# Optimization experiments

Hardware: AMD Instinct MI355X
Metric: run time of the kernel (lower is better)

Reference implementation:

```python
import jax, jax.numpy as jnp
import numpy as np

B, N = 2048, 64
Q_SIZE, K_SIZE, HIDDEN, OUT_SIZE, N_HEAD = 512, 512, 128, 512, 8
LN_EPS = 1e-5


def setup_inputs() -> dict:
    key = jax.random.key(0)
    ks = jax.random.split(key, 9)
    s_q = 1.0 / np.sqrt(Q_SIZE)
    s_k = 1.0 / np.sqrt(K_SIZE)
    s_o = 1.0 / np.sqrt(N_HEAD * HIDDEN)
    return {
        "me": jax.random.normal(ks[0], (B, Q_SIZE), jnp.float32),
        "other": jax.random.normal(ks[1], (B, N, K_SIZE), jnp.float32),
        # stacked per-head projection weights (torch Linear applied as x @ W)
        "Wq": jax.random.normal(ks[2], (N_HEAD, Q_SIZE, HIDDEN), jnp.float32) * s_q,
        "bq": jnp.zeros((N_HEAD, HIDDEN), jnp.float32),
        "Wk": jax.random.normal(ks[3], (N_HEAD, K_SIZE, HIDDEN), jnp.float32) * s_k,
        "Wv": jax.random.normal(ks[4], (N_HEAD, K_SIZE, HIDDEN), jnp.float32) * s_k,
        "gamma": jnp.ones((N_HEAD * HIDDEN,), jnp.float32),
        "beta": jnp.zeros((N_HEAD * HIDDEN,), jnp.float32),
        "Wo": jax.random.normal(ks[5], (N_HEAD * HIDDEN, OUT_SIZE), jnp.float32) * s_o,
    }


def _mhat2(me, other, Wq, bq, Wk, Wv, gamma, beta, Wo):
    # per-head projections, batched over the head axis
    q = jnp.einsum("bq,hqd->bhd", me, Wq) + bq[None]          # [B,H,D]
    k = jnp.einsum("bnk,hkd->bhnd", other, Wk)                 # [B,H,N,D]
    v = jnp.einsum("bnk,hkd->bhnd", other, Wv)                 # [B,H,N,D]
    scale = 1.0 / jnp.sqrt(jnp.asarray(HIDDEN, me.dtype))
    a = jnp.einsum("bhd,bhnd->bhn", q, k) * scale              # [B,H,N]
    a = jax.nn.softmax(a, axis=-1)
    out = jnp.einsum("bhn,bhnd->bhd", a, v)                    # [B,H,D]
    c = out.reshape(out.shape[0], N_HEAD * HIDDEN)             # concat heads
    mu = jnp.mean(c, axis=-1, keepdims=True)
    var = jnp.mean(jnp.square(c - mu), axis=-1, keepdims=True)
    cn = (c - mu) * jax.lax.rsqrt(var + LN_EPS) * gamma + beta
    return jax.nn.relu(cn) @ Wo                                # [B,OUT]


def reference(me, other, Wq, bq, Wk, Wv, gamma, beta, Wo):
    return _mhat2(me, other, Wq, bq, Wk, Wv, gamma, beta, Wo)
```

## Files before the change

### kernel.cpp

```cpp
#include <hip/hip_runtime.h>
#include <math.h>

typedef __attribute__((ext_vector_type(4))) float f32x4;
typedef __attribute__((ext_vector_type(4))) unsigned int u32x4;
typedef __attribute__((ext_vector_type(8))) short s16x8;

#define SCALE_INV_SQRT_H 0.08838834764831845f

__device__ __forceinline__ unsigned short f2bf(float x){
  unsigned int u = __builtin_bit_cast(unsigned int, x);
  u += 0x7fffu + ((u >> 16) & 1u);
  return (unsigned short)(u >> 16);
}
__device__ __forceinline__ float bf2f(unsigned short s){
  unsigned int u = ((unsigned int)s) << 16;
  return __builtin_bit_cast(float, u);
}

__device__ __forceinline__ void gemm_core(
    const unsigned short* __restrict__ Ag, int lda,
    const unsigned short* __restrict__ Bg, int ldb,
    int ksteps, unsigned short* As, unsigned short* Bs, f32x4 acc[4][4])
{
  const int t = threadIdx.x, lane = t & 63, w = t >> 6;
  const int m0 = (w >> 1) * 64, n0 = (w & 1) * 64;
  const int r = t >> 1, u0 = (t & 1) * 4;
  for (int kk = 0; kk < ksteps; kk++) {
    __syncthreads();
    const unsigned short* ga = Ag + (size_t)r * lda + kk * 64;
    const unsigned short* gb = Bg + (size_t)r * ldb + kk * 64;
#pragma unroll
    for (int q = 0; q < 4; q++) {
      u32x4 va = *(const u32x4*)(ga + (u0 + q) * 8);
      u32x4 vb = *(const u32x4*)(gb + (u0 + q) * 8);
      ((u32x4*)(As + r * 64))[(u0 + q) ^ (r & 7)] = va;
      ((u32x4*)(Bs + r * 64))[(u0 + q) ^ (r & 7)] = vb;
    }
    __syncthreads();
    s16x8 af[4][2], bfr[4][2];
#pragma unroll
    for (int i = 0; i < 4; i++) {
#pragma unroll
      for (int ks = 0; ks < 2; ks++) {
        int ra = m0 + i * 16 + (lane & 15);
        int sa = ks * 4 + (lane >> 4);
        af[i][ks] = *(const s16x8*)(As + ra * 64 + ((sa ^ (ra & 7)) << 3));
        int rb = n0 + i * 16 + (lane & 15);
        bfr[i][ks] = *(const s16x8*)(Bs + rb * 64 + ((sa ^ (rb & 7)) << 3));
      }
    }
#pragma unroll
    for (int ks = 0; ks < 2; ks++)
#pragma unroll
      for (int i = 0; i < 4; i++)
#pragma unroll
        for (int j = 0; j < 4; j++)
          acc[i][j] = __builtin_amdgcn_mfma_f32_16x16x32_bf16(af[i][ks], bfr[j][ks], acc[i][j], 0, 0, 0);
  }
}

__device__ __forceinline__ void store_bf16_tile(unsigned short* __restrict__ C, int ldc, f32x4 acc[4][4]){
  const int t = threadIdx.x, lane = t & 63, w = t >> 6;
  const int m0 = (w >> 1) * 64, n0 = (w & 1) * 64;
#pragma unroll
  for (int i = 0; i < 4; i++)
#pragma unroll
    for (int j = 0; j < 4; j++) {
      int col = n0 + j * 16 + (lane & 15);
#pragma unroll
      for (int rg = 0; rg < 4; rg++) {
        int row = m0 + i * 16 + (lane >> 4) * 4 + rg;
        C[(size_t)row * ldc + col] = f2bf(acc[i][j][rg]);
      }
    }
}

__device__ __forceinline__ void transpose_tile(const float* __restrict__ src, int lda,
                                               unsigned short* __restrict__ dst, int ldb,
                                               int r0, int c0, unsigned short (*tile)[72])
{
  const int t = threadIdx.x;
  const int cc = (t & 15) * 4, rr = t >> 4;
#pragma unroll
  for (int j = 0; j < 4; j++) {
    int r = rr + j * 16;
    f32x4 v = *(const f32x4*)(src + (size_t)(r0 + r) * lda + c0 + cc);
#pragma unroll
    for (int q = 0; q < 4; q++) tile[r][cc + q] = f2bf(v[q]);
  }
  __syncthreads();
  const int c = t >> 2, rb = (t & 3) * 16;
  unsigned short o[16];
#pragma unroll
  for (int q = 0; q < 16; q++) o[q] = tile[rb + q][c];
  u32x4 p0, p1;
#pragma unroll
  for (int q = 0; q < 4; q++) {
    p0[q] = (unsigned)o[2 * q]     | ((unsigned)o[2 * q + 1] << 16);
    p1[q] = (unsigned)o[2 * q + 8] | ((unsigned)o[2 * q + 9] << 16);
  }
  unsigned short* dp = dst + (size_t)(c0 + c) * ldb + r0 + rb;
  *(u32x4*)dp = p0;
  *(u32x4*)(dp + 8) = p1;
}

__global__ __launch_bounds__(256) void k_conv(
  const float* __restrict__ me, const float* __restrict__ Wq, const float* __restrict__ Wk,
  const float* __restrict__ Wv, const float* __restrict__ Wo,
  unsigned short* __restrict__ me_b, unsigned short* __restrict__ wk_b,
  unsigned short* __restrict__ wqt, unsigned short* __restrict__ wvt,
  unsigned short* __restrict__ wot)
{
  __shared__ unsigned short tile[64][72];
  const int bid = blockIdx.x, t = threadIdx.x;
  if (bid < 256) {
    for (int v = bid * 256 + t; v < 393216; v += 256 * 256) {
      const float* sp; unsigned short* dp;
      if (v < 262144) { sp = me + 4 * (size_t)v; dp = me_b + 4 * (size_t)v; }
      else { int i = v - 262144; sp = Wk + 4 * (size_t)i; dp = wk_b + 4 * (size_t)i; }
      f32x4 x = *(const f32x4*)sp;
      unsigned long long pk = (unsigned long long)((unsigned)f2bf(x[0]) | ((unsigned)f2bf(x[1]) << 16))
                            | (((unsigned long long)((unsigned)f2bf(x[2]) | ((unsigned)f2bf(x[3]) << 16))) << 32);
      *(unsigned long long*)dp = pk;
    }
    return;
  }
  if (bid < 384) {
    int idx = bid - 256, h = idx >> 4, tl = idx & 15;
    transpose_tile(Wq + (size_t)h * 65536, 128, wqt + (size_t)h * 65536, 512,
                   (tl >> 1) * 64, (tl & 1) * 64, tile);
  } else if (bid < 512) {
    int idx = bid - 384, h = idx >> 4, tl = idx & 15;
    transpose_tile(Wv + (size_t)h * 65536, 128, wvt + (size_t)h * 65536, 512,
                   (tl >> 1) * 64, (tl & 1) * 64, tile);
  } else {
    int idx = bid - 512;
    transpose_tile(Wo, 512, wot, 1024, (idx >> 3) * 64, (idx & 7) * 64, tile);
  }
}

__global__ __launch_bounds__(256) void k_q(const unsigned short* __restrict__ me_b,
                                           const unsigned short* __restrict__ wqt,
                                           const float* __restrict__ bq,
                                           unsigned short* __restrict__ q_b)
{
  __shared__ unsigned short As[128 * 64], Bs[128 * 64];
  int bid = blockIdx.x;
  int bm = bid >> 3, bn = bid & 7;
  f32x4 acc[4][4]; f32x4 z = {0.f, 0.f, 0.f, 0.f};
#pragma unroll
  for (int i = 0; i < 4; i++) for (int j = 0; j < 4; j++) acc[i][j] = z;
  gemm_core(me_b + (size_t)bm * 128 * 512, 512, wqt + (size_t)bn * 65536, 512, 8, As, Bs, acc);
  const int t = threadIdx.x, lane = t & 63, w = t >> 6;
  const int m0 = (w >> 1) * 64, n0 = (w & 1) * 64;
#pragma unroll
  for (int i = 0; i < 4; i++)
#pragma unroll
    for (int j = 0; j < 4; j++) {
      int col = bn * 128 + n0 + j * 16 + (lane & 15);
      float bqv = bq[col];
#pragma unroll
      for (int rg = 0; rg < 4; rg++) {
        int row = bm * 128 + m0 + i * 16 + (lane >> 4) * 4 + rg;
        q_b[(size_t)row * 1024 + col] = f2bf(acc[i][j][rg] + bqv);
      }
    }
}

__global__ __launch_bounds__(256) void k_u(const unsigned short* __restrict__ q_b,
                                           const unsigned short* __restrict__ wk_b,
                                           unsigned short* __restrict__ T)
{
  __shared__ unsigned short As[128 * 64], Bs[128 * 64];
  int bid = blockIdx.x;
  int h = bid >> 6, bm = (bid >> 2) & 15, bn = bid & 3;
  f32x4 acc[4][4]; f32x4 z = {0.f, 0.f, 0.f, 0.f};
#pragma unroll
  for (int i = 0; i < 4; i++) for (int j = 0; j < 4; j++) acc[i][j] = z;
  gemm_core(q_b + (size_t)bm * 128 * 1024 + h * 128, 1024,
            wk_b + (size_t)h * 65536 + bn * 16384, 128, 2, As, Bs, acc);
  const int t = threadIdx.x, lane = t & 63, w = t >> 6;
  const int m0 = (w >> 1) * 64, n0 = (w & 1) * 64;
#pragma unroll
  for (int i = 0; i < 4; i++)
#pragma unroll
    for (int j = 0; j < 4; j++) {
      int col = h * 512 + bn * 128 + n0 + j * 16 + (lane & 15);
#pragma unroll
      for (int rg = 0; rg < 4; rg++) {
        int row = bm * 128 + m0 + i * 16 + (lane >> 4) * 4 + rg;
        T[(size_t)row * 4096 + col] = f2bf(acc[i][j][rg] * SCALE_INV_SQRT_H);
      }
    }
}

__global__ __launch_bounds__(256) void k_attn(const float* __restrict__ other,
                                              const unsigned short* __restrict__ T,
                                              unsigned short* __restrict__ wbuf)
{
  __shared__ unsigned short oth[64 * 512];
  __shared__ unsigned short t_lds[8 * 512];
  __shared__ float s_lds[8 * 66];
  __shared__ char a_raw[4 * 1056];
  const int b = blockIdx.x;
  const int t = threadIdx.x, l = t & 63, w = t >> 6;

  {
    int row = t >> 5;
    int col0 = (t & 31) * 16;
    const unsigned short* gp = T + (size_t)b * 4096 + row * 512 + col0;
#pragma unroll
    for (int i = 0; i < 2; i++) {
      u32x4 v = *(const u32x4*)(gp + i * 8);
      int gr = (col0 >> 3) + i;
      *(u32x4*)((char*)t_lds + row * 1024 + ((gr ^ row) << 4)) = v;
    }
  }
  {
    int n = t >> 2;
    int nx = n & 7;
    const f32x4* gp = (const f32x4*)(other + (size_t)b * 32768 + (size_t)n * 512);
#pragma unroll
    for (int j0 = 0; j0 < 32; j0 += 8) {
      f32x4 v[8];
#pragma unroll
      for (int jj = 0; jj < 8; jj++) v[jj] = gp[(t & 3) + (j0 + jj) * 4];
#pragma unroll
      for (int jj = 0; jj < 8; jj++) {
        int kf0 = (t & 3) * 4 + (j0 + jj) * 16;
        unsigned int lo = (unsigned)f2bf(v[jj][0]) | ((unsigned)f2bf(v[jj][1]) << 16);
        unsigned int hi = (unsigned)f2bf(v[jj][2]) | ((unsigned)f2bf(v[jj][3]) << 16);
        unsigned long long pk = (unsigned long long)lo | ((unsigned long long)hi << 32);
        int g = kf0 >> 3;
        *(unsigned long long*)((char*)oth + n * 1024 + ((g ^ nx) << 4) + (kf0 & 7) * 2) = pk;
      }
    }
  }
  __syncthreads();

  {
    f32x4 sacc = {0.f, 0.f, 0.f, 0.f};
    int arow = l & 7;
    int bn = w * 16 + (l & 15);
    int bx = bn & 7;
#pragma unroll
    for (int kk = 0; kk < 16; kk++) {
      int gr = kk * 4 + (l >> 4);
      s16x8 af  = *(const s16x8*)((char*)t_lds + arow * 1024 + ((gr ^ arow) << 4));
      s16x8 bfv = *(const s16x8*)((char*)oth + bn * 1024 + ((gr ^ bx) << 4));
      sacc = __builtin_amdgcn_mfma_f32_16x16x32_bf16(af, bfv, sacc, 0, 0, 0);
    }
    int hbase = (l >> 4) * 4;
    if (hbase < 8) {
#pragma unroll
      for (int rg = 0; rg < 4; rg++) s_lds[(hbase + rg) * 66 + w * 16 + (l & 15)] = sacc[rg];
    }
  }
  __syncthreads();

#pragma unroll
  for (int hh = 0; hh < 2; hh++) {
    int h = w * 2 + hh;
    float v = s_lds[h * 66 + l];
    float mx = v;
#pragma unroll
    for (int off = 32; off > 0; off >>= 1) mx = fmaxf(mx, __shfl_xor(mx, off));
    float p = __expf(v - mx);
    float sm = p;
#pragma unroll
    for (int off = 32; off > 0; off >>= 1) sm += __shfl_xor(sm, off);
    unsigned short ab = f2bf(p / sm);
#pragma unroll
    for (int rep = 0; rep < 4; rep++)
      *(unsigned short*)(a_raw + rep * 1056 + h * 128 + l * 2) = ab;
  }
  __syncthreads();

  {
    int g = l >> 4;
    int klane = l & 15;
    int kf0 = w * 128 + klane * 8;
    const char* abase = a_raw + g * 1056;
    s16x8 a0[8], a1[8];
#pragma unroll
    for (int r = 0; r < 8; r++) {
      a0[r] = *(const s16x8*)(abase + (2 * g) * 128 + r * 16);
      a1[r] = *(const s16x8*)(abase + (2 * g + 1) * 128 + r * 16);
    }
    float acc0[8], acc1[8];
#pragma unroll
    for (int q = 0; q < 8; q++) { acc0[q] = 0.f; acc1[q] = 0.f; }
    const char* obase = (const char*)oth;
    int gsl = w * 16 + klane;
#pragma unroll
    for (int r = 0; r < 8; r++) {
#pragma unroll
      for (int jj = 0; jj < 8; jj++) {
        int n = r * 8 + jj;
        float av0 = bf2f((unsigned short)a0[r][jj]);
        float av1 = bf2f((unsigned short)a1[r][jj]);
        s16x8 o = *(const s16x8*)(obase + n * 1024 + ((gsl ^ (n & 7)) << 4));
#pragma unroll
        for (int q = 0; q < 8; q++) {
          float f = bf2f((unsigned short)o[q]);
          acc0[q] += av0 * f;
          acc1[q] += av1 * f;
        }
      }
    }
    int h0 = 2 * g, h1 = h0 + 1;
    u32x4 p0, p1;
#pragma unroll
    for (int q = 0; q < 4; q++) {
      p0[q] = (unsigned)f2bf(acc0[2 * q]) | ((unsigned)f2bf(acc0[2 * q + 1]) << 16);
      p1[q] = (unsigned)f2bf(acc1[2 * q]) | ((unsigned)f2bf(acc1[2 * q + 1]) << 16);
    }
    *(u32x4*)(wbuf + ((size_t)b * 8 + h0) * 512 + kf0) = p0;
    *(u32x4*)(wbuf + ((size_t)b * 8 + h1) * 512 + kf0) = p1;
  }
}

__global__ __launch_bounds__(256) void k_c(const unsigned short* __restrict__ wbuf,
                                           const unsigned short* __restrict__ wvt,
                                           unsigned short* __restrict__ cbuf)
{
  __shared__ unsigned short As[128 * 64], Bs[128 * 64];
  int bid = blockIdx.x;
  int bm = bid >> 3, h = bid & 7;
  f32x4 acc[4][4]; f32x4 z = {0.f, 0.f, 0.f, 0.f};
#pragma unroll
  for (int i = 0; i < 4; i++) for (int j = 0; j < 4; j++) acc[i][j] = z;
  gemm_core(wbuf + ((size_t)bm * 128 * 8 + h) * 512, 4096, wvt + (size_t)h * 65536, 512, 8, As, Bs, acc);
  store_bf16_tile(cbuf + (size_t)bm * 128 * 1024 + h * 128, 1024, acc);
}

__global__ __launch_bounds__(256) void k_out(const unsigned short* __restrict__ cbuf,
                                             const float* __restrict__ gamma,
                                             const float* __restrict__ beta,
                                             const unsigned short* __restrict__ wot,
                                             float* __restrict__ out)
{
  __shared__ unsigned short As[32 * 1024];
  __shared__ unsigned short Bs[128 * 64];
  int bid = blockIdx.x;
  int bm = bid >> 2, bn = bid & 3;
  const int t = threadIdx.x, lane = t & 63, w = t >> 6;
  {
    int r = t >> 3;
    const unsigned short* g = cbuf + (size_t)(bm * 32 + r) * 1024;
#pragma unroll
    for (int q = 0; q < 16; q++) {
      int u = (t & 7) + q * 8;
      u32x4 v = *(const u32x4*)(g + u * 8);
      ((u32x4*)(As + r * 1024))[u ^ (r & 7)] = v;
    }
  }
  float gv[16], bv[16];
#pragma unroll
  for (int si = 0; si < 2; si++)
#pragma unroll
    for (int j = 0; j < 8; j++) {
      int k = (lane + si * 64) * 8 + j;
      gv[si * 8 + j] = gamma[k];
      bv[si * 8 + j] = beta[k];
    }
  __syncthreads();
  for (int rr = 0; rr < 8; rr++) {
    int r = w * 8 + rr;
    float vals[16]; float sum = 0.f, sq = 0.f;
#pragma unroll
    for (int si = 0; si < 2; si++) {
      int s = lane + si * 64;
      s16x8 pv = *(const s16x8*)(As + r * 1024 + ((s ^ (r & 7)) << 3));
#pragma unroll
      for (int j = 0; j < 8; j++) { float f = bf2f((unsigned short)pv[j]); vals[si * 8 + j] = f; sum += f; sq += f * f; }
    }
#pragma unroll
    for (int off = 32; off > 0; off >>= 1) { sum += __shfl_xor(sum, off); sq += __shfl_xor(sq, off); }
    float mu = sum * (1.f / 1024.f);
    float var = sq * (1.f / 1024.f) - mu * mu;
    float rs = rsqrtf(var + 1e-5f);
#pragma unroll
    for (int si = 0; si < 2; si++) {
      int s = lane + si * 64;
      unsigned short o[8];
#pragma unroll
      for (int j = 0; j < 8; j++) {
        float f = (vals[si * 8 + j] - mu) * rs * gv[si * 8 + j] + bv[si * 8 + j];
        o[j] = f2bf(fmaxf(f, 0.f));
      }
      u32x4 pk;
      pk[0] = (unsigned)o[0] | ((unsigned)o[1] << 16);
      pk[1] = (unsigned)o[2] | ((unsigned)o[3] << 16);
      pk[2] = (unsigned)o[4] | ((unsigned)o[5] << 16);
      pk[3] = (unsigned)o[6] | ((unsigned)o[7] << 16);
      ((u32x4*)(As + r * 1024))[s ^ (r & 7)] = pk;
    }
  }
  const int wm = w >> 1, wn = w & 1;
  f32x4 acc[4]; f32x4 z = {0.f, 0.f, 0.f, 0.f};
#pragma unroll
  for (int j = 0; j < 4; j++) acc[j] = z;
  const unsigned short* Bg = wot + (size_t)bn * 128 * 1024;
  const int rB = t >> 1, u0 = (t & 1) * 4;
  for (int kk = 0; kk < 16; kk++) {
    __syncthreads();
#pragma unroll
    for (int q = 0; q < 4; q++) {
      u32x4 vb = *(const u32x4*)(Bg + (size_t)rB * 1024 + kk * 64 + (u0 + q) * 8);
      ((u32x4*)(Bs + rB * 64))[(u0 + q) ^ (rB & 7)] = vb;
    }
    __syncthreads();
#pragma unroll
    for (int ks = 0; ks < 2; ks++) {
      int ra = wm * 16 + (lane & 15);
      int sa = kk * 8 + ks * 4 + (lane >> 4);
      s16x8 af = *(const s16x8*)(As + ra * 1024 + ((sa ^ (ra & 7)) << 3));
#pragma unroll
      for (int j = 0; j < 4; j++) {
        int rb = wn * 64 + j * 16 + (lane & 15);
        int sb = ks * 4 + (lane >> 4);
        s16x8 bfv = *(const s16x8*)(Bs + rb * 64 + ((sb ^ (rb & 7)) << 3));
        acc[j] = __builtin_amdgcn_mfma_f32_16x16x32_bf16(af, bfv, acc[j], 0, 0, 0);
      }
    }
  }
#pragma unroll
  for (int j = 0; j < 4; j++) {
    int col = bn * 128 + wn * 64 + j * 16 + (lane & 15);
#pragma unroll
    for (int rg = 0; rg < 4; rg++) {
      int row = bm * 32 + wm * 16 + (lane >> 4) * 4 + rg;
      out[(size_t)row * 512 + col] = acc[j][rg];
    }
  }
}

extern "C" void kernel_launch(void* const* d_in, const int* in_sizes, int n_in,
                              void* d_out, int out_size, void* d_ws, size_t ws_size,
                              hipStream_t stream)
{
  (void)in_sizes; (void)n_in; (void)out_size;
  const float* me    = (const float*)d_in[0];
  const float* other = (const float*)d_in[1];
  const float* Wq    = (const float*)d_in[2];
  const float* bq    = (const float*)d_in[3];
  const float* Wk    = (const float*)d_in[4];
  const float* Wv    = (const float*)d_in[5];
  const float* gamma = (const float*)d_in[6];
  const float* beta  = (const float*)d_in[7];
  const float* Wo    = (const float*)d_in[8];
  float* out = (float*)d_out;
  char* ws = (char*)d_ws;

  unsigned short* me_b = (unsigned short*)(ws + 0);
  unsigned short* wk_b = (unsigned short*)(ws + 2097152);
  unsigned short* wqt  = (unsigned short*)(ws + 3145728);
  unsigned short* wvt  = (unsigned short*)(ws + 4194304);
  unsigned short* wot  = (unsigned short*)(ws + 5242880);
  unsigned short* q_b  = (unsigned short*)(ws + 6291456);
  unsigned short* T_b  = (unsigned short*)(ws + 10485760);
  unsigned short* w_b  = (unsigned short*)(ws + 27262976);
  unsigned short* c_b  = (unsigned short*)(ws + 44040192);
  if (ws_size < 48234496) return;

  k_conv<<<dim3(640),  dim3(256), 0, stream>>>(me, Wq, Wk, Wv, Wo, me_b, wk_b, wqt, wvt, wot);
  k_q   <<<dim3(128),  dim3(256), 0, stream>>>(me_b, wqt, bq, q_b);
  k_u   <<<dim3(512),  dim3(256), 0, stream>>>(q_b, wk_b, T_b);
  k_attn<<<dim3(2048), dim3(256), 0, stream>>>(other, T_b, w_b);
  k_c   <<<dim3(128),  dim3(256), 0, stream>>>(w_b, wvt, c_b);
  k_out <<<dim3(256),  dim3(256), 0, stream>>>(c_b, gamma, beta, wot, out);
}
```

Before: 129.9 us.

## Fuse Q and U GEMMs and software-pipeline attention over four batches per block

Merges the q projection and the q·Wk^T product into one kernel that keeps the Q tile in LDS, removing the q_b round trip and one launch. Each block now recomputes the Q tile for its head (four times across the bn tiles), which adds redundant compute. The attention kernel now processes four batch rows per block, prefetching the next row's `other`/T data into registers while the current row computes. It also splits the `other` conversion into two halves so the first QK MFMAs can start early. Barriers are replaced by an lgkmcnt wait plus s_barrier, and occupancy is pinned with launch_bounds(256,2), which raises register pressure from the 16-register prefetch buffer.

```diff
diff --git a/kernel.cpp b/kernel.cpp
--- a/kernel.cpp
+++ b/kernel.cpp
@@ -15,6 +15,11 @@
 __device__ __forceinline__ float bf2f(unsigned short s){
   unsigned int u = ((unsigned int)s) << 16;
   return __builtin_bit_cast(float, u);
+}
+
+__device__ __forceinline__ void bar_lds(){
+  asm volatile("s_waitcnt lgkmcnt(0)" ::: "memory");
+  __builtin_amdgcn_s_barrier();
 }
 
 __device__ __forceinline__ void gemm_core(
@@ -139,48 +144,73 @@
   }
 }
 
-__global__ __launch_bounds__(256) void k_q(const unsigned short* __restrict__ me_b,
-                                           const unsigned short* __restrict__ wqt,
-                                           const float* __restrict__ bq,
-                                           unsigned short* __restrict__ q_b)
-{
-  __shared__ unsigned short As[128 * 64], Bs[128 * 64];
+__global__ __launch_bounds__(256) void k_qu(const unsigned short* __restrict__ me_b,
+                                            const unsigned short* __restrict__ wqt,
+                                            const float* __restrict__ bq,
+                                            const unsigned short* __restrict__ wk_b,
+                                            unsigned short* __restrict__ T)
+{
+  __shared__ unsigned short St[2][128 * 64];
+  __shared__ unsigned short Qs[128 * 128];
   int bid = blockIdx.x;
-  int bm = bid >> 3, bn = bid & 7;
-  f32x4 acc[4][4]; f32x4 z = {0.f, 0.f, 0.f, 0.f};
-#pragma unroll
-  for (int i = 0; i < 4; i++) for (int j = 0; j < 4; j++) acc[i][j] = z;
-  gemm_core(me_b + (size_t)bm * 128 * 512, 512, wqt + (size_t)bn * 65536, 512, 8, As, Bs, acc);
+  int swz = (bid & 7) * 64 + (bid >> 3);
+  int bm = swz >> 5, h = (swz >> 2) & 7, bn = swz & 3;
   const int t = threadIdx.x, lane = t & 63, w = t >> 6;
   const int m0 = (w >> 1) * 64, n0 = (w & 1) * 64;
+
+  f32x4 qacc[4][4]; f32x4 z = {0.f, 0.f, 0.f, 0.f};
+#pragma unroll
+  for (int i = 0; i < 4; i++) for (int j = 0; j < 4; j++) qacc[i][j] = z;
+  gemm_core(me_b + (size_t)bm * 128 * 512, 512, wqt + (size_t)h * 65536, 512, 8, St[0], St[1], qacc);
 #pragma unroll
   for (int i = 0; i < 4; i++)
 #pragma unroll
     for (int j = 0; j < 4; j++) {
-      int col = bn * 128 + n0 + j * 16 + (lane & 15);
-      float bqv = bq[col];
+      int col = n0 + j * 16 + (lane & 15);
+      float bqv = bq[h * 128 + col];
 #pragma unroll
       for (int rg = 0; rg < 4; rg++) {
-        int row = bm * 128 + m0 + i * 16 + (lane >> 4) * 4 + rg;
-        q_b[(size_t)row * 1024 + col] = f2bf(acc[i][j][rg] + bqv);
-      }
-    }
-}
-
-__global__ __launch_bounds__(256) void k_u(const unsigned short* __restrict__ q_b,
-                                           const unsigned short* __restrict__ wk_b,
-                                           unsigned short* __restrict__ T)
-{
-  __shared__ unsigned short As[128 * 64], Bs[128 * 64];
-  int bid = blockIdx.x;
-  int h = bid >> 6, bm = (bid >> 2) & 15, bn = bid & 3;
-  f32x4 acc[4][4]; f32x4 z = {0.f, 0.f, 0.f, 0.f};
+        int row = m0 + i * 16 + (lane >> 4) * 4 + rg;
+        *(unsigned short*)((char*)Qs + row * 256 + ((((col >> 3) ^ (row & 15)) << 4)) + (col & 7) * 2)
+            = f2bf(qacc[i][j][rg] + bqv);
+      }
+    }
+  __syncthreads();
+  {
+    const int r = t >> 1, u0 = (t & 1) * 4;
+    const unsigned short* gb = wk_b + (size_t)h * 65536 + (size_t)(bn * 128 + r) * 128;
+#pragma unroll
+    for (int kt = 0; kt < 2; kt++)
+#pragma unroll
+      for (int q = 0; q < 4; q++) {
+        u32x4 vb = *(const u32x4*)(gb + kt * 64 + (u0 + q) * 8);
+        ((u32x4*)(St[kt] + r * 64))[(u0 + q) ^ (r & 7)] = vb;
+      }
+  }
+  __syncthreads();
+  f32x4 acc[4][4];
 #pragma unroll
   for (int i = 0; i < 4; i++) for (int j = 0; j < 4; j++) acc[i][j] = z;
-  gemm_core(q_b + (size_t)bm * 128 * 1024 + h * 128, 1024,
-            wk_b + (size_t)h * 65536 + bn * 16384, 128, 2, As, Bs, acc);
-  const int t = threadIdx.x, lane = t & 63, w = t >> 6;
-  const int m0 = (w >> 1) * 64, n0 = (w & 1) * 64;
+#pragma unroll
+  for (int kt = 0; kt < 2; kt++)
+#pragma unroll
+    for (int ks = 0; ks < 2; ks++) {
+      s16x8 af[4], bf[4];
+#pragma unroll
+      for (int i = 0; i < 4; i++) {
+        int ra = m0 + i * 16 + (lane & 15);
+        int gq = (kt * 2 + ks) * 4 + (lane >> 4);
+        af[i] = *(const s16x8*)((char*)Qs + ra * 256 + ((gq ^ (ra & 15)) << 4));
+        int rb = n0 + i * 16 + (lane & 15);
+        int sa = ks * 4 + (lane >> 4);
+        bf[i] = *(const s16x8*)(St[kt] + rb * 64 + ((sa ^ (rb & 7)) << 3));
+      }
+#pragma unroll
+      for (int i = 0; i < 4; i++)
+#pragma unroll
+        for (int j = 0; j < 4; j++)
+          acc[i][j] = __builtin_amdgcn_mfma_f32_16x16x32_bf16(af[i], bf[j], acc[i][j], 0, 0, 0);
+    }
 #pragma unroll
   for (int i = 0; i < 4; i++)
 #pragma unroll
@@ -194,129 +224,165 @@
     }
 }
 
-__global__ __launch_bounds__(256) void k_attn(const float* __restrict__ other,
-                                              const unsigned short* __restrict__ T,
-                                              unsigned short* __restrict__ wbuf)
+__global__ __launch_bounds__(256, 2) void k_attn(const float* __restrict__ other,
+                                                 const unsigned short* __restrict__ T,
+                                                 unsigned short* __restrict__ wbuf)
 {
   __shared__ unsigned short oth[64 * 512];
   __shared__ unsigned short t_lds[8 * 512];
   __shared__ float s_lds[8 * 66];
   __shared__ char a_raw[4 * 1056];
-  const int b = blockIdx.x;
   const int t = threadIdx.x, l = t & 63, w = t >> 6;
+  const int b0 = blockIdx.x * 4;
+
+  const int n = t >> 2;
+  const int nx = n & 7;
+  const int c4 = (t & 3) * 4;
+  const int trow = t >> 5;
+  const int tcol0 = (t & 31) * 16;
+
+  f32x4 pf[16];
+  u32x4 tv[2];
 
   {
-    int row = t >> 5;
-    int col0 = (t & 31) * 16;
-    const unsigned short* gp = T + (size_t)b * 4096 + row * 512 + col0;
+    const f32x4* gp = (const f32x4*)(other + (size_t)b0 * 32768 + (size_t)n * 512);
+#pragma unroll
+    for (int j = 0; j < 16; j++) pf[j] = gp[(t & 3) + j * 4];
+    const unsigned short* tp = T + (size_t)b0 * 4096 + trow * 512 + tcol0;
+#pragma unroll
+    for (int i = 0; i < 2; i++) tv[i] = *(const u32x4*)(tp + i * 8);
+  }
+
+  for (int it = 0; it < 4; it++) {
+    const int b = b0 + it;
+#pragma unroll
+    for (int j = 0; j < 16; j++) {
+      int kf0 = c4 + j * 16;
+      unsigned int lo = (unsigned)f2bf(pf[j][0]) | ((unsigned)f2bf(pf[j][1]) << 16);
+      unsigned int hi = (unsigned)f2bf(pf[j][2]) | ((unsigned)f2bf(pf[j][3]) << 16);
+      unsigned long long pk = (unsigned long long)lo | ((unsigned long long)hi << 32);
+      int g = kf0 >> 3;
+      *(unsigned long long*)((char*)oth + n * 1024 + ((g ^ nx) << 4) + (kf0 & 7) * 2) = pk;
+    }
 #pragma unroll
     for (int i = 0; i < 2; i++) {
-      u32x4 v = *(const u32x4*)(gp + i * 8);
-      int gr = (col0 >> 3) + i;
-      *(u32x4*)((char*)t_lds + row * 1024 + ((gr ^ row) << 4)) = v;
-    }
-  }
-  {
-    int n = t >> 2;
-    int nx = n & 7;
-    const f32x4* gp = (const f32x4*)(other + (size_t)b * 32768 + (size_t)n * 512);
-#pragma unroll
-    for (int j0 = 0; j0 < 32; j0 += 8) {
-      f32x4 v[8];
-#pragma unroll
-      for (int jj = 0; jj < 8; jj++) v[jj] = gp[(t & 3) + (j0 + jj) * 4];
-#pragma unroll
-      for (int jj = 0; jj < 8; jj++) {
-        int kf0 = (t & 3) * 4 + (j0 + jj) * 16;
-        unsigned int lo = (unsigned)f2bf(v[jj][0]) | ((unsigned)f2bf(v[jj][1]) << 16);
-        unsigned int hi = (unsigned)f2bf(v[jj][2]) | ((unsigned)f2bf(v[jj][3]) << 16);
-        unsigned long long pk = (unsigned long long)lo | ((unsigned long long)hi << 32);
-        int g = kf0 >> 3;
-        *(unsigned long long*)((char*)oth + n * 1024 + ((g ^ nx) << 4) + (kf0 & 7) * 2) = pk;
-      }
-    }
-  }
-  __syncthreads();
-
-  {
+      int gr = (tcol0 >> 3) + i;
+      *(u32x4*)((char*)t_lds + trow * 1024 + ((gr ^ trow) << 4)) = tv[i];
+    }
+    {
+      const f32x4* gp = (const f32x4*)(other + (size_t)b * 32768 + (size_t)n * 512 + 256);
+#pragma unroll
+      for (int j = 0; j < 16; j++) pf[j] = gp[(t & 3) + j * 4];
+    }
+    bar_lds();
+
     f32x4 sacc = {0.f, 0.f, 0.f, 0.f};
-    int arow = l & 7;
-    int bn = w * 16 + (l & 15);
-    int bx = bn & 7;
-#pragma unroll
-    for (int kk = 0; kk < 16; kk++) {
+    const int arow = l & 7;
+    const int g1n = w * 16 + (l & 15);
+    const int g1x = g1n & 7;
+#pragma unroll
+    for (int kk = 0; kk < 8; kk++) {
       int gr = kk * 4 + (l >> 4);
       s16x8 af  = *(const s16x8*)((char*)t_lds + arow * 1024 + ((gr ^ arow) << 4));
-      s16x8 bfv = *(const s16x8*)((char*)oth + bn * 1024 + ((gr ^ bx) << 4));
+      s16x8 bfv = *(const s16x8*)((char*)oth + g1n * 1024 + ((gr ^ g1x) << 4));
       sacc = __builtin_amdgcn_mfma_f32_16x16x32_bf16(af, bfv, sacc, 0, 0, 0);
     }
-    int hbase = (l >> 4) * 4;
-    if (hbase < 8) {
-#pragma unroll
-      for (int rg = 0; rg < 4; rg++) s_lds[(hbase + rg) * 66 + w * 16 + (l & 15)] = sacc[rg];
-    }
-  }
-  __syncthreads();
-
-#pragma unroll
-  for (int hh = 0; hh < 2; hh++) {
-    int h = w * 2 + hh;
-    float v = s_lds[h * 66 + l];
-    float mx = v;
-#pragma unroll
-    for (int off = 32; off > 0; off >>= 1) mx = fmaxf(mx, __shfl_xor(mx, off));
-    float p = __expf(v - mx);
-    float sm = p;
-#pragma unroll
-    for (int off = 32; off > 0; off >>= 1) sm += __shfl_xor(sm, off);
-    unsigned short ab = f2bf(p / sm);
-#pragma unroll
-    for (int rep = 0; rep < 4; rep++)
-      *(unsigned short*)(a_raw + rep * 1056 + h * 128 + l * 2) = ab;
-  }
-  __syncthreads();
-
-  {
-    int g = l >> 4;
-    int klane = l & 15;
-    int kf0 = w * 128 + klane * 8;
-    const char* abase = a_raw + g * 1056;
-    s16x8 a0[8], a1[8];
-#pragma unroll
-    for (int r = 0; r < 8; r++) {
-      a0[r] = *(const s16x8*)(abase + (2 * g) * 128 + r * 16);
-      a1[r] = *(const s16x8*)(abase + (2 * g + 1) * 128 + r * 16);
-    }
-    float acc0[8], acc1[8];
-#pragma unroll
-    for (int q = 0; q < 8; q++) { acc0[q] = 0.f; acc1[q] = 0.f; }
-    const char* obase = (const char*)oth;
-    int gsl = w * 16 + klane;
-#pragma unroll
-    for (int r = 0; r < 8; r++) {
-#pragma unroll
-      for (int jj = 0; jj < 8; jj++) {
-        int n = r * 8 + jj;
-        float av0 = bf2f((unsigned short)a0[r][jj]);
-        float av1 = bf2f((unsigned short)a1[r][jj]);
-        s16x8 o = *(const s16x8*)(obase + n * 1024 + ((gsl ^ (n & 7)) << 4));
-#pragma unroll
-        for (int q = 0; q < 8; q++) {
-          float f = bf2f((unsigned short)o[q]);
-          acc0[q] += av0 * f;
-          acc1[q] += av1 * f;
+#pragma unroll
+    for (int j = 0; j < 16; j++) {
+      int kf0 = 256 + c4 + j * 16;
+      unsigned int lo = (unsigned)f2bf(pf[j][0]) | ((unsigned)f2bf(pf[j][1]) << 16);
+      unsigned int hi = (unsigned)f2bf(pf[j][2]) | ((unsigned)f2bf(pf[j][3]) << 16);
+      unsigned long long pk = (unsigned long long)lo | ((unsigned long long)hi << 32);
+      int g = kf0 >> 3;
+      *(unsigned long long*)((char*)oth + n * 1024 + ((g ^ nx) << 4) + (kf0 & 7) * 2) = pk;
+    }
+    bar_lds();
+
+#pragma unroll
+    for (int kk = 8; kk < 16; kk++) {
+      int gr = kk * 4 + (l >> 4);
+      s16x8 af  = *(const s16x8*)((char*)t_lds + arow * 1024 + ((gr ^ arow) << 4));
+      s16x8 bfv = *(const s16x8*)((char*)oth + g1n * 1024 + ((gr ^ g1x) << 4));
+      sacc = __builtin_amdgcn_mfma_f32_16x16x32_bf16(af, bfv, sacc, 0, 0, 0);
+    }
+    if (it < 3) {
+      const f32x4* gp = (const f32x4*)(other + (size_t)(b + 1) * 32768 + (size_t)n * 512);
+#pragma unroll
+      for (int j = 0; j < 16; j++) pf[j] = gp[(t & 3) + j * 4];
+      const unsigned short* tp = T + (size_t)(b + 1) * 4096 + trow * 512 + tcol0;
+#pragma unroll
+      for (int i = 0; i < 2; i++) tv[i] = *(const u32x4*)(tp + i * 8);
+    }
+    {
+      int hbase = (l >> 4) * 4;
+      if (hbase < 8) {
+#pragma unroll
+        for (int rg = 0; rg < 4; rg++) s_lds[(hbase + rg) * 66 + w * 16 + (l & 15)] = sacc[rg];
+      }
+    }
+    bar_lds();
+
+#pragma unroll
+    for (int hh = 0; hh < 2; hh++) {
+      int h = w * 2 + hh;
+      float v = s_lds[h * 66 + l];
+      float mx = v;
+#pragma unroll
+      for (int off = 32; off > 0; off >>= 1) mx = fmaxf(mx, __shfl_xor(mx, off));
+      float p = __expf(v - mx);
+      float sm = p;
+#pragma unroll
+      for (int off = 32; off > 0; off >>= 1) sm += __shfl_xor(sm, off);
+      unsigned short ab = f2bf(p / sm);
+#pragma unroll
+      for (int rep = 0; rep < 4; rep++)
+        *(unsigned short*)(a_raw + rep * 1056 + h * 128 + l * 2) = ab;
+    }
+    bar_lds();
+
+    {
+      int g = l >> 4;
+      int klane = l & 15;
+      int kf0 = w * 128 + klane * 8;
+      const char* abase = a_raw + g * 1056;
+      s16x8 a0[8], a1[8];
+#pragma unroll
+      for (int r = 0; r < 8; r++) {
+        a0[r] = *(const s16x8*)(abase + (2 * g) * 128 + r * 16);
+        a1[r] = *(const s16x8*)(abase + (2 * g + 1) * 128 + r * 16);
+      }
+      float acc0[8], acc1[8];
+#pragma unroll
+      for (int q = 0; q < 8; q++) { acc0[q] = 0.f; acc1[q] = 0.f; }
+      const char* obase = (const char*)oth;
+      int gsl = w * 16 + klane;
+#pragma unroll
+      for (int r = 0; r < 8; r++) {
+#pragma unroll
+        for (int jj = 0; jj < 8; jj++) {
+          int nn = r * 8 + jj;
+          float av0 = bf2f((unsigned short)a0[r][jj]);
+          float av1 = bf2f((unsigned short)a1[r][jj]);
+          s16x8 o = *(const s16x8*)(obase + nn * 1024 + ((gsl ^ (nn & 7)) << 4));
+#pragma unroll
+          for (int q = 0; q < 8; q++) {
+            float f = bf2f((unsigned short)o[q]);
+            acc0[q] += av0 * f;
+            acc1[q] += av1 * f;
+          }
         }
       }
-    }
-    int h0 = 2 * g, h1 = h0 + 1;
-    u32x4 p0, p1;
-#pragma unroll
-    for (int q = 0; q < 4; q++) {
-      p0[q] = (unsigned)f2bf(acc0[2 * q]) | ((unsigned)f2bf(acc0[2 * q + 1]) << 16);
-      p1[q] = (unsigned)f2bf(acc1[2 * q]) | ((unsigned)f2bf(acc1[2 * q + 1]) << 16);
-    }
-    *(u32x4*)(wbuf + ((size_t)b * 8 + h0) * 512 + kf0) = p0;
-    *(u32x4*)(wbuf + ((size_t)b * 8 + h1) * 512 + kf0) = p1;
+      int h0 = 2 * g, h1 = h0 + 1;
+      u32x4 p0, p1;
+#pragma unroll
+      for (int q = 0; q < 4; q++) {
+        p0[q] = (unsigned)f2bf(acc0[2 * q]) | ((unsigned)f2bf(acc0[2 * q + 1]) << 16);
+        p1[q] = (unsigned)f2bf(acc1[2 * q]) | ((unsigned)f2bf(acc1[2 * q + 1]) << 16);
+      }
+      *(u32x4*)(wbuf + ((size_t)b * 8 + h0) * 512 + kf0) = p0;
+      *(u32x4*)(wbuf + ((size_t)b * 8 + h1) * 512 + kf0) = p1;
+    }
+    bar_lds();
   }
 }
 
@@ -458,16 +524,14 @@
   unsigned short* wqt  = (unsigned short*)(ws + 3145728);
   unsigned short* wvt  = (unsigned short*)(ws + 4194304);
   unsigned short* wot  = (unsigned short*)(ws + 5242880);
-  unsigned short* q_b  = (unsigned short*)(ws + 6291456);
   unsigned short* T_b  = (unsigned short*)(ws + 10485760);
   unsigned short* w_b  = (unsigned short*)(ws + 27262976);
   unsigned short* c_b  = (unsigned short*)(ws + 44040192);
   if (ws_size < 48234496) return;
 
   k_conv<<<dim3(640),  dim3(256), 0, stream>>>(me, Wq, Wk, Wv, Wo, me_b, wk_b, wqt, wvt, wot);
-  k_q   <<<dim3(128),  dim3(256), 0, stream>>>(me_b, wqt, bq, q_b);
-  k_u   <<<dim3(512),  dim3(256), 0, stream>>>(q_b, wk_b, T_b);
-  k_attn<<<dim3(2048), dim3(256), 0, stream>>>(other, T_b, w_b);
+  k_qu  <<<dim3(512),  dim3(256), 0, stream>>>(me_b, wqt, bq, wk_b, T_b);
+  k_attn<<<dim3(512),  dim3(256), 0, stream>>>(other, T_b, w_b);
   k_c   <<<dim3(128),  dim3(256), 0, stream>>>(w_b, wvt, c_b);
   k_out <<<dim3(256),  dim3(256), 0, stream>>>(c_b, gamma, beta, wot, out);
 }
```

Result: slower. 172.0 us (+32.4%).

## Fuse Q projection and K-absorption GEMMs into one kernel; lighten attn barriers

Applied to the files above, without the earlier changes.

Merges the q projection kernel and the q·Wk^T kernel into a single kernel. Each block computes its 128x128 q tile for one head, keeps it in swizzled LDS, then multiplies by a preloaded Wk slice, so the q_b round trip through global memory and one launch go away. The cost is that the q GEMM is recomputed four times, once per bn block. The attention kernel also replaces __syncthreads with a barrier that only waits on LDS counters, dropping the wait on outstanding global memory operations.

```diff
diff --git a/kernel.cpp b/kernel.cpp
--- a/kernel.cpp
+++ b/kernel.cpp
@@ -15,6 +15,11 @@
 __device__ __forceinline__ float bf2f(unsigned short s){
   unsigned int u = ((unsigned int)s) << 16;
   return __builtin_bit_cast(float, u);
+}
+
+__device__ __forceinline__ void bar_lds(){
+  asm volatile("s_waitcnt lgkmcnt(0)" ::: "memory");
+  __builtin_amdgcn_s_barrier();
 }
 
 __device__ __forceinline__ void gemm_core(
@@ -139,48 +144,73 @@
   }
 }
 
-__global__ __launch_bounds__(256) void k_q(const unsigned short* __restrict__ me_b,
-                                           const unsigned short* __restrict__ wqt,
-                                           const float* __restrict__ bq,
-                                           unsigned short* __restrict__ q_b)
-{
-  __shared__ unsigned short As[128 * 64], Bs[128 * 64];
+__global__ __launch_bounds__(256) void k_qu(const unsigned short* __restrict__ me_b,
+                                            const unsigned short* __restrict__ wqt,
+                                            const float* __restrict__ bq,
+                                            const unsigned short* __restrict__ wk_b,
+                                            unsigned short* __restrict__ T)
+{
+  __shared__ unsigned short St[2][128 * 64];
+  __shared__ unsigned short Qs[128 * 128];
   int bid = blockIdx.x;
-  int bm = bid >> 3, bn = bid & 7;
-  f32x4 acc[4][4]; f32x4 z = {0.f, 0.f, 0.f, 0.f};
-#pragma unroll
-  for (int i = 0; i < 4; i++) for (int j = 0; j < 4; j++) acc[i][j] = z;
-  gemm_core(me_b + (size_t)bm * 128 * 512, 512, wqt + (size_t)bn * 65536, 512, 8, As, Bs, acc);
+  int swz = (bid & 7) * 64 + (bid >> 3);
+  int bm = swz >> 5, h = (swz >> 2) & 7, bn = swz & 3;
   const int t = threadIdx.x, lane = t & 63, w = t >> 6;
   const int m0 = (w >> 1) * 64, n0 = (w & 1) * 64;
+
+  f32x4 qacc[4][4]; f32x4 z = {0.f, 0.f, 0.f, 0.f};
+#pragma unroll
+  for (int i = 0; i < 4; i++) for (int j = 0; j < 4; j++) qacc[i][j] = z;
+  gemm_core(me_b + (size_t)bm * 128 * 512, 512, wqt + (size_t)h * 65536, 512, 8, St[0], St[1], qacc);
 #pragma unroll
   for (int i = 0; i < 4; i++)
 #pragma unroll
     for (int j = 0; j < 4; j++) {
-      int col = bn * 128 + n0 + j * 16 + (lane & 15);
-      float bqv = bq[col];
+      int col = n0 + j * 16 + (lane & 15);
+      float bqv = bq[h * 128 + col];
 #pragma unroll
       for (int rg = 0; rg < 4; rg++) {
-        int row = bm * 128 + m0 + i * 16 + (lane >> 4) * 4 + rg;
-        q_b[(size_t)row * 1024 + col] = f2bf(acc[i][j][rg] + bqv);
-      }
-    }
-}
-
-__global__ __launch_bounds__(256) void k_u(const unsigned short* __restrict__ q_b,
-                                           const unsigned short* __restrict__ wk_b,
-                                           unsigned short* __restrict__ T)
-{
-  __shared__ unsigned short As[128 * 64], Bs[128 * 64];
-  int bid = blockIdx.x;
-  int h = bid >> 6, bm = (bid >> 2) & 15, bn = bid & 3;
-  f32x4 acc[4][4]; f32x4 z = {0.f, 0.f, 0.f, 0.f};
+        int row = m0 + i * 16 + (lane >> 4) * 4 + rg;
+        *(unsigned short*)((char*)Qs + row * 256 + ((((col >> 3) ^ (row & 15)) << 4)) + (col & 7) * 2)
+            = f2bf(qacc[i][j][rg] + bqv);
+      }
+    }
+  __syncthreads();
+  {
+    const int r = t >> 1, u0 = (t & 1) * 4;
+    const unsigned short* gb = wk_b + (size_t)h * 65536 + (size_t)(bn * 128 + r) * 128;
+#pragma unroll
+    for (int kt = 0; kt < 2; kt++)
+#pragma unroll
+      for (int q = 0; q < 4; q++) {
+        u32x4 vb = *(const u32x4*)(gb + kt * 64 + (u0 + q) * 8);
+        ((u32x4*)(St[kt] + r * 64))[(u0 + q) ^ (r & 7)] = vb;
+      }
+  }
+  __syncthreads();
+  f32x4 acc[4][4];
 #pragma unroll
   for (int i = 0; i < 4; i++) for (int j = 0; j < 4; j++) acc[i][j] = z;
-  gemm_core(q_b + (size_t)bm * 128 * 1024 + h * 128, 1024,
-            wk_b + (size_t)h * 65536 + bn * 16384, 128, 2, As, Bs, acc);
-  const int t = threadIdx.x, lane = t & 63, w = t >> 6;
-  const int m0 = (w >> 1) * 64, n0 = (w & 1) * 64;
+#pragma unroll
+  for (int kt = 0; kt < 2; kt++)
+#pragma unroll
+    for (int ks = 0; ks < 2; ks++) {
+      s16x8 af[4], bf[4];
+#pragma unroll
+      for (int i = 0; i < 4; i++) {
+        int ra = m0 + i * 16 + (lane & 15);
+        int gq = (kt * 2 + ks) * 4 + (lane >> 4);
+        af[i] = *(const s16x8*)((char*)Qs + ra * 256 + ((gq ^ (ra & 15)) << 4));
+        int rb = n0 + i * 16 + (lane & 15);
+        int sa = ks * 4 + (lane >> 4);
+        bf[i] = *(const s16x8*)(St[kt] + rb * 64 + ((sa ^ (rb & 7)) << 3));
+      }
+#pragma unroll
+      for (int i = 0; i < 4; i++)
+#pragma unroll
+        for (int j = 0; j < 4; j++)
+          acc[i][j] = __builtin_amdgcn_mfma_f32_16x16x32_bf16(af[i], bf[j], acc[i][j], 0, 0, 0);
+    }
 #pragma unroll
   for (int i = 0; i < 4; i++)
 #pragma unroll
@@ -236,7 +266,7 @@
       }
     }
   }
-  __syncthreads();
+  bar_lds();
 
   {
     f32x4 sacc = {0.f, 0.f, 0.f, 0.f};
@@ -256,7 +286,7 @@
       for (int rg = 0; rg < 4; rg++) s_lds[(hbase + rg) * 66 + w * 16 + (l & 15)] = sacc[rg];
     }
   }
-  __syncthreads();
+  bar_lds();
 
 #pragma unroll
   for (int hh = 0; hh < 2; hh++) {
@@ -274,7 +304,7 @@
     for (int rep = 0; rep < 4; rep++)
       *(unsigned short*)(a_raw + rep * 1056 + h * 128 + l * 2) = ab;
   }
-  __syncthreads();
+  bar_lds();
 
   {
     int g = l >> 4;
@@ -458,15 +488,13 @@
   unsigned short* wqt  = (unsigned short*)(ws + 3145728);
   unsigned short* wvt  = (unsigned short*)(ws + 4194304);
   unsigned short* wot  = (unsigned short*)(ws + 5242880);
-  unsigned short* q_b  = (unsigned short*)(ws + 6291456);
   unsigned short* T_b  = (unsigned short*)(ws + 10485760);
   unsigned short* w_b  = (unsigned short*)(ws + 27262976);
   unsigned short* c_b  = (unsigned short*)(ws + 44040192);
   if (ws_size < 48234496) return;
 
   k_conv<<<dim3(640),  dim3(256), 0, stream>>>(me, Wq, Wk, Wv, Wo, me_b, wk_b, wqt, wvt, wot);
-  k_q   <<<dim3(128),  dim3(256), 0, stream>>>(me_b, wqt, bq, q_b);
-  k_u   <<<dim3(512),  dim3(256), 0, stream>>>(q_b, wk_b, T_b);
+  k_qu  <<<dim3(512),  dim3(256), 0, stream>>>(me_b, wqt, bq, wk_b, T_b);
   k_attn<<<dim3(2048), dim3(256), 0, stream>>>(other, T_b, w_b);
   k_c   <<<dim3(128),  dim3(256), 0, stream>>>(w_b, wvt, c_b);
   k_out <<<dim3(256),  dim3(256), 0, stream>>>(c_b, gamma, beta, wot, out);
```

Result: faster. 126.0 us (-3.0%).
